# Optimization experiments

Measured on AMD Instinct MI355X. Metric: run time of the kernel, lower is better.

Reference implementation:

```python
import jax, jax.numpy as jnp
import numpy as np

N = 100000   # nodes
E = 1600000  # edges (pos and neg each)
F_IN = 256
H = 64       # hidden == out_dim


def setup_inputs() -> dict:
    key = jax.random.key(0)
    ks = jax.random.split(key, 12)
    x = jax.random.normal(ks[0], (N, F_IN), dtype=jnp.float32)
    edge_index = jax.random.randint(ks[1], (2, E), 0, N, dtype=jnp.int64)
    neg_edge_index = jax.random.randint(ks[2], (2, E), 0, N, dtype=jnp.int64)
    s = 0.05
    return {
        "x": x,
        "edge_index": edge_index,
        "neg_edge_index": neg_edge_index,
        "W1": jax.random.normal(ks[3], (F_IN, H), dtype=jnp.float32) * s,
        "b1": jnp.zeros((H,), jnp.float32),
        "W2": jax.random.normal(ks[4], (H, H), dtype=jnp.float32) * s,
        "b2": jnp.zeros((H,), jnp.float32),
        "Wp1": jax.random.normal(ks[5], (2 * H, 128), dtype=jnp.float32) * s,
        "bp1": jnp.zeros((128,), jnp.float32),
        "Wp2": jax.random.normal(ks[6], (128, 64), dtype=jnp.float32) * s,
        "bp2": jnp.zeros((64,), jnp.float32),
        "Wp3": jax.random.normal(ks[7], (64, 1), dtype=jnp.float32) * s,
        "bp3": jnp.zeros((1,), jnp.float32),
    }


def gcn_conv(x, edge_index, W, b):
    # PyG GCNConv: add self-loops, symmetric normalization D^-1/2 (A+I) D^-1/2, x@W + b
    xw = x @ W  # [N,H]
    loop = jnp.arange(N, dtype=edge_index.dtype)
    src = jnp.concatenate([edge_index[0], loop])
    dst = jnp.concatenate([edge_index[1], loop])
    deg = jax.ops.segment_sum(jnp.ones(src.shape[0], xw.dtype), dst, num_segments=N)
    dinv = jnp.where(deg > 0, jax.lax.rsqrt(jnp.maximum(deg, 1e-12)), 0.0)
    norm = dinv[src] * dinv[dst]  # [E+N]
    msgs = xw[src] * norm[:, None]
    out = jax.ops.segment_sum(msgs, dst, num_segments=N)
    return out + b


def predict_link(z, edge_index, Wp1, bp1, Wp2, bp2, Wp3, bp3):
    src, dst = edge_index[0], edge_index[1]
    # cat([z[src], z[dst]]) @ Wp1 == z[src] @ Wp1[:H] + z[dst] @ Wp1[H:]
    h = jnp.maximum(z[src] @ Wp1[:H] + z[dst] @ Wp1[H:] + bp1, 0.0)
    h = jnp.maximum(h @ Wp2 + bp2, 0.0)
    return (h @ Wp3 + bp3)[:, 0]


def reference(x, edge_index, neg_edge_index, W1, b1, W2, b2, Wp1, bp1, Wp2, bp2, Wp3, bp3):
    # encode (dropout inactive: eval mode)
    z = jnp.maximum(gcn_conv(x, edge_index, W1, b1), 0.0)
    z = jnp.maximum(gcn_conv(z, edge_index, W2, b2), 0.0)
    pos = predict_link(z, edge_index, Wp1, bp1, Wp2, bp2, Wp3, bp3)
    neg = predict_link(z, neg_edge_index, Wp1, bp1, Wp2, bp2, Wp3, bp3)
    return pos, neg, z
```

## Files before the change

### kernel.cpp

```cpp
#include <hip/hip_runtime.h>
#include <hip/hip_bf16.h>

#define NODES 100000
#define SCAN_B 200
#define CHUNK 500

typedef __attribute__((ext_vector_type(4))) float f4v;
typedef __attribute__((ext_vector_type(8))) short bfx8;
typedef __attribute__((ext_vector_type(4))) float f32x4;
typedef unsigned short ushort_t;
typedef unsigned int uint_t;

__device__ __forceinline__ ushort_t f2b(float f) {
  union { float f; uint_t u; } v; v.f = f;
  return (ushort_t)((v.u + 0x7fffu + ((v.u >> 16) & 1u)) >> 16);
}
__device__ __forceinline__ float b2f(ushort_t h) {
  union { uint_t u; float f; } v; v.u = ((uint_t)h) << 16;
  return v.f;
}
__device__ __forceinline__ uint_t pk2(float a, float b) {
  union { __hip_bfloat16 h; ushort_t u; } lo, hi;
  lo.h = __float2bfloat16(a);
  hi.h = __float2bfloat16(b);
  return (uint_t)lo.u | ((uint_t)hi.u << 16);
}

__device__ __forceinline__ int permn1(int r) {
  int t = r >> 4, g = (r >> 2) & 3, p = (r >> 1) & 1, e = r & 1;
  int w = 2 * (t & 1) + p;
  return 32 * (t >> 1) + 8 * (g ^ w) + 2 * w + e;
}

#define MFMA16(A, B, C) __builtin_amdgcn_mfma_f32_16x16x32_bf16((A), (B), (C), 0, 0, 0)


__global__ void count_deg(const int* __restrict__ dst, int* __restrict__ deg, int E) {
  int i = blockIdx.x * 256 + threadIdx.x;
  if (i < E) atomicAdd(&deg[dst[i]], 1);
}

__global__ void dinv_k(const int* __restrict__ deg, float* __restrict__ dinv, int n) {
  int i = blockIdx.x * 256 + threadIdx.x;
  if (i < n) dinv[i] = 1.0f / sqrtf((float)(deg[i] + 1));
}

__global__ void scan_sum(const int* __restrict__ deg, int* __restrict__ bsum) {
  __shared__ int sh[256];
  int b = blockIdx.x, t = threadIdx.x;
  int base = b * CHUNK;
  int v = 0;
  for (int i = t; i < CHUNK; i += 256) v += deg[base + i];
  sh[t] = v;
  __syncthreads();
  for (int s = 128; s > 0; s >>= 1) {
    if (t < s) sh[t] += sh[t + s];
    __syncthreads();
  }
  if (t == 0) bsum[b] = sh[0];
}

__global__ void scan_top(int* __restrict__ bsum) {
  __shared__ int sh[SCAN_B];
  int t = threadIdx.x;
  if (t < SCAN_B) sh[t] = bsum[t];
  __syncthreads();
  if (t == 0) {
    int run = 0;
    for (int i = 0; i < SCAN_B; ++i) { int x = sh[i]; sh[i] = run; run += x; }
  }
  __syncthreads();
  if (t < SCAN_B) bsum[t] = sh[t];
}

__global__ void scan_out(const int* __restrict__ deg, const int* __restrict__ bsum,
                         int* __restrict__ row_start, int E) {
  __shared__ int sh[CHUNK];
  int b = blockIdx.x, t = threadIdx.x;
  int base = b * CHUNK;
  for (int i = t; i < CHUNK; i += 256) sh[i] = deg[base + i];
  __syncthreads();
  if (t == 0) {
    int run = bsum[b];
    for (int i = 0; i < CHUNK; ++i) { int x = sh[i]; sh[i] = run; run += x; }
  }
  __syncthreads();
  for (int i = t; i < CHUNK; i += 256) row_start[base + i] = sh[i];
  if (b == SCAN_B - 1 && t == 0) row_start[NODES] = E;
}

__global__ void fill_csr(const int* __restrict__ src, const int* __restrict__ dst,
                         const int* __restrict__ row_start, int* __restrict__ cursor,
                         int* __restrict__ csr, int E) {
  int i = blockIdx.x * 256 + threadIdx.x;
  if (i < E) {
    int d = dst[i];
    int p = atomicAdd(&cursor[d], 1);
    csr[row_start[d] + p] = src[i];
  }
}

template <int K>
__global__ __launch_bounds__(256) void conv_gemm(
    const float* __restrict__ A, const float* __restrict__ W,
    const float* __restrict__ dinv, float* __restrict__ out, int n) {
  constexpr int KT = K / 32;
  constexpr int SEGS = K / 8;
  __shared__ __align__(16) ushort_t lhi[32 * K];
  __shared__ __align__(16) ushort_t llo[32 * K];

  int tid = threadIdx.x;
  int lane = tid & 63, wave = tid >> 6;
  int q = lane & 15, g = lane >> 4;
  int c0 = wave * 16;
  int r0 = blockIdx.x * 32;

  bfx8 bhi[KT], blo[KT];
#pragma unroll
  for (int kt = 0; kt < KT; ++kt) {
    bfx8 h, l;
#pragma unroll
    for (int j = 0; j < 8; ++j) {
      float w = W[(size_t)(kt * 32 + g * 8 + j) * 64 + c0 + q];
      ushort_t hb = f2b(w);
      float lo = w - b2f(hb);
      h[j] = (short)hb;
      l[j] = (short)f2b(lo);
    }
    bhi[kt] = h;
    blo[kt] = l;
  }

  for (int idx = tid; idx < 32 * SEGS; idx += 256) {
    int row = idx / SEGS, s = idx % SEGS;
    const float* p = A + (size_t)(r0 + row) * K + s * 8;
    f4v v0 = *(const f4v*)p;
    f4v v1 = *(const f4v*)(p + 4);
    bfx8 h8, l8;
#pragma unroll
    for (int j = 0; j < 4; ++j) {
      ushort_t hb = f2b(v0[j]);
      h8[j] = (short)hb;
      l8[j] = (short)f2b(v0[j] - b2f(hb));
      ushort_t hb1 = f2b(v1[j]);
      h8[4 + j] = (short)hb1;
      l8[4 + j] = (short)f2b(v1[j] - b2f(hb1));
    }
    int boff = row * (K * 2) + ((s * 16) ^ ((row & 7) << 4));
    *(bfx8*)((char*)lhi + boff) = h8;
    *(bfx8*)((char*)llo + boff) = l8;
  }
  __syncthreads();

  f32x4 hh[2], hl[2], lh[2];
#pragma unroll
  for (int rt = 0; rt < 2; ++rt) {
    hh[rt] = (f32x4){0.f, 0.f, 0.f, 0.f};
    hl[rt] = (f32x4){0.f, 0.f, 0.f, 0.f};
    lh[rt] = (f32x4){0.f, 0.f, 0.f, 0.f};
  }
#pragma unroll
  for (int kt = 0; kt < KT; ++kt) {
#pragma unroll
    for (int rt = 0; rt < 2; ++rt) {
      int row = rt * 16 + q;
      int boff = row * (K * 2) + (((kt * 64 + g * 16)) ^ ((row & 7) << 4));
      bfx8 ah = *(const bfx8*)((const char*)lhi + boff);
      bfx8 al = *(const bfx8*)((const char*)llo + boff);
      hh[rt] = MFMA16(ah, bhi[kt], hh[rt]);
      hl[rt] = MFMA16(ah, blo[kt], hl[rt]);
      lh[rt] = MFMA16(al, bhi[kt], lh[rt]);
    }
  }

#pragma unroll
  for (int rt = 0; rt < 2; ++rt) {
    f32x4 s = hh[rt] + hl[rt] + lh[rt];
#pragma unroll
    for (int j = 0; j < 4; ++j) {
      int row = r0 + rt * 16 + g * 4 + j;
      if (row < n) out[(size_t)row * 64 + c0 + q] = s[j] * dinv[row];
    }
  }
}

__global__ void agg_k(const float* __restrict__ P, const int* __restrict__ row_start,
                      const int* __restrict__ csr, const float* __restrict__ dinv,
                      const float* __restrict__ bias, float* __restrict__ out,
                      ushort_t* __restrict__ zb, int n) {
  int wave = threadIdx.x >> 6, lane = threadIdx.x & 63;
  int i = blockIdx.x * 4 + wave;
  if (i >= n) return;
  const float* Pl = P + lane;
  float a0 = Pl[(size_t)i * 64];
  float a1 = 0.f, a2 = 0.f, a3 = 0.f;
  int beg = row_start[i], end = row_start[i + 1];
  int j = beg;
  for (; j + 8 <= end; j += 8) {
    int s0 = csr[j + 0], s1 = csr[j + 1], s2 = csr[j + 2], s3 = csr[j + 3];
    int s4 = csr[j + 4], s5 = csr[j + 5], s6 = csr[j + 6], s7 = csr[j + 7];
    float v0 = Pl[(size_t)s0 * 64];
    float v1 = Pl[(size_t)s1 * 64];
    float v2 = Pl[(size_t)s2 * 64];
    float v3 = Pl[(size_t)s3 * 64];
    float v4 = Pl[(size_t)s4 * 64];
    float v5 = Pl[(size_t)s5 * 64];
    float v6 = Pl[(size_t)s6 * 64];
    float v7 = Pl[(size_t)s7 * 64];
    a0 += v0; a1 += v1; a2 += v2; a3 += v3;
    a0 += v4; a1 += v5; a2 += v6; a3 += v7;
  }
  if (j + 4 <= end) {
    int s0 = csr[j + 0], s1 = csr[j + 1], s2 = csr[j + 2], s3 = csr[j + 3];
    float v0 = Pl[(size_t)s0 * 64];
    float v1 = Pl[(size_t)s1 * 64];
    float v2 = Pl[(size_t)s2 * 64];
    float v3 = Pl[(size_t)s3 * 64];
    a0 += v0; a1 += v1; a2 += v2; a3 += v3;
    j += 4;
  }
  for (; j < end; ++j) a1 += Pl[(size_t)csr[j] * 64];
  float acc = (a0 + a1) + (a2 + a3);
  float v = fmaxf(acc * dinv[i] + bias[lane], 0.0f);
  out[(size_t)i * 64 + lane] = v;
  if (zb) zb[(size_t)i * 64 + lane] = f2b(v);
}

__global__ __launch_bounds__(1024) void mlp_kernel(
    const int* __restrict__ ei, const ushort_t* __restrict__ zb,
    const float* __restrict__ Wp1, const float* __restrict__ bp1,
    const float* __restrict__ Wp2, const float* __restrict__ bp2,
    const float* __restrict__ Wp3, const float* __restrict__ bp3,
    float* __restrict__ out, int E) {
  __shared__ __align__(16) char WT1[32768];
  __shared__ __align__(16) char WF2[16384];
  __shared__ __align__(16) float Lb1[128];
  __shared__ __align__(16) float Lb2[64];
  __shared__ __align__(16) float Lw3[64];

  int tid = threadIdx.x;
  int lane = tid & 63, wave = tid >> 6;
  int q = lane & 15, g = lane >> 4;

  for (int idx = tid; idx < 2048; idx += 1024) {
    int l = idx & 63, f = idx >> 6;
    int t = f & 7, kk = f >> 3;
    int lq = l & 15, lg = l >> 4;
    int n1 = permn1(t * 16 + lq);
    bfx8 v;
#pragma unroll
    for (int j = 0; j < 8; ++j)
      v[j] = (short)f2b(Wp1[(kk * 32 + lg * 8 + j) * 128 + n1]);
    *(bfx8*)(WT1 + idx * 16) = v;
  }
  for (int idx = tid; idx < 1024; idx += 1024) {
    int l = idx & 63, fk = idx >> 6;
    int t2 = fk >> 2, kk = fk & 3;
    int lq = l & 15, lg = l >> 4;
    bfx8 v;
#pragma unroll
    for (int j = 0; j < 8; ++j)
      v[j] = (short)f2b(Wp2[(kk * 32 + lg * 8 + j) * 64 + t2 * 16 + lq]);
    *(bfx8*)(WF2 + idx * 16) = v;
  }
  if (tid < 128) Lb1[tid] = bp1[permn1(tid)];
  if (tid < 64) { Lb2[tid] = bp2[tid]; Lw3[tid] = Wp3[tid]; }
  __syncthreads();

  float bp3v = bp3[0];

  int nbt = E >> 8;
  int bt0 = blockIdx.x << 2;
  int ewq = (wave << 4) + q;

  int si[6], di[6];
  bfx8 af[4], afn[4];

  {
    int e = ((bt0 + 0) < nbt) ? (((bt0 + 0) << 8) + ewq) : 0;
    si[0] = ei[e]; di[0] = ei[E + e];
  }
  {
    int e = ((bt0 + 1) < nbt) ? (((bt0 + 1) << 8) + ewq) : 0;
    si[1] = ei[e]; di[1] = ei[E + e];
  }
#pragma unroll
  for (int kk = 0; kk < 4; ++kk) {
    int node = (kk < 2) ? si[0] : di[0];
    af[kk] = *(const bfx8*)(zb + (size_t)node * 64 + ((kk & 1) << 5) + (g << 3));
  }

#pragma unroll
  for (int it = 0; it < 4; ++it) {
    if (bt0 + it < nbt) {
      if (it + 2 < 4) {
        int e = ((bt0 + it + 2) < nbt) ? (((bt0 + it + 2) << 8) + ewq) : 0;
        si[it + 2] = ei[e]; di[it + 2] = ei[E + e];
      }
      if (it + 1 < 4 && (bt0 + it + 1) < nbt) {
#pragma unroll
        for (int kk = 0; kk < 4; ++kk) {
          int node = (kk < 2) ? si[it + 1] : di[it + 1];
          afn[kk] = *(const bfx8*)(zb + (size_t)node * 64 + ((kk & 1) << 5) + (g << 3));
        }
      } else {
#pragma unroll
        for (int kk = 0; kk < 4; ++kk) afn[kk] = af[kk];
      }

      f32x4 acc2[4];
#pragma unroll
      for (int t2 = 0; t2 < 4; ++t2) acc2[t2] = (f32x4){0.f, 0.f, 0.f, 0.f};

#pragma unroll
      for (int m = 0; m < 4; ++m) {
        f32x4 a0 = (f32x4){0.f, 0.f, 0.f, 0.f};
        f32x4 a1 = (f32x4){0.f, 0.f, 0.f, 0.f};
#pragma unroll
        for (int kk = 0; kk < 4; ++kk) {
          bfx8 wf0 = *(const bfx8*)(WT1 + ((kk * 8 + 2 * m) * 64 + lane) * 16);
          bfx8 wf1 = *(const bfx8*)(WT1 + ((kk * 8 + 2 * m + 1) * 64 + lane) * 16);
          a0 = MFMA16(wf0, af[kk], a0);
          a1 = MFMA16(wf1, af[kk], a1);
        }
        f4v bv0 = *(const f4v*)(Lb1 + (2 * m) * 16 + g * 4);
        f4v bv1 = *(const f4v*)(Lb1 + (2 * m + 1) * 16 + g * 4);
        bfx8 wf2[4];
#pragma unroll
        for (int t2 = 0; t2 < 4; ++t2)
          wf2[t2] = *(const bfx8*)(WF2 + ((t2 * 4 + m) * 64 + lane) * 16);
        uint_t c0 = pk2(fmaxf(a0[0] + bv0[0], 0.f), fmaxf(a0[1] + bv0[1], 0.f));
        uint_t c1 = pk2(fmaxf(a0[2] + bv0[2], 0.f), fmaxf(a0[3] + bv0[3], 0.f));
        uint_t c2 = pk2(fmaxf(a1[0] + bv1[0], 0.f), fmaxf(a1[1] + bv1[1], 0.f));
        uint_t c3 = pk2(fmaxf(a1[2] + bv1[2], 0.f), fmaxf(a1[3] + bv1[3], 0.f));
        uint_t d1 = __shfl_xor(c1, 16, 64);
        uint_t d2 = __shfl_xor(c2, 32, 64);
        uint_t d3 = __shfl_xor(c3, 48, 64);
        union { uint_t u[4]; bfx8 v; } hf;
        hf.u[0] = c0; hf.u[1] = d1; hf.u[2] = d2; hf.u[3] = d3;
#pragma unroll
        for (int t2 = 0; t2 < 4; ++t2)
          acc2[t2] = MFMA16(wf2[t2], hf.v, acc2[t2]);
      }

      float sacc = 0.f;
#pragma unroll
      for (int t2 = 0; t2 < 4; ++t2) {
        f4v b2v = *(const f4v*)(Lb2 + t2 * 16 + g * 4);
        f4v w3v = *(const f4v*)(Lw3 + t2 * 16 + g * 4);
#pragma unroll
        for (int j = 0; j < 4; ++j) {
          float h = fmaxf(acc2[t2][j] + b2v[j], 0.f);
          sacc = fmaf(h, w3v[j], sacc);
        }
      }
      sacc += __shfl_xor(sacc, 16, 64);
      sacc += __shfl_xor(sacc, 32, 64);
      if (g == 0) out[((bt0 + it) << 8) + ewq] = sacc + bp3v;

#pragma unroll
      for (int kk = 0; kk < 4; ++kk) af[kk] = afn[kk];
    }
  }
}


static inline size_t alup(size_t x) { return (x + 511) & ~(size_t)511; }

extern "C" void kernel_launch(void* const* d_in, const int* in_sizes, int n_in,
                              void* d_out, int out_size, void* d_ws, size_t ws_size,
                              hipStream_t stream) {
  const float* x = (const float*)d_in[0];
  const int* ei = (const int*)d_in[1];
  const int* nei = (const int*)d_in[2];
  const float* W1 = (const float*)d_in[3];
  const float* b1 = (const float*)d_in[4];
  const float* W2 = (const float*)d_in[5];
  const float* b2 = (const float*)d_in[6];
  const float* Wp1 = (const float*)d_in[7];
  const float* bp1 = (const float*)d_in[8];
  const float* Wp2 = (const float*)d_in[9];
  const float* bp2 = (const float*)d_in[10];
  const float* Wp3 = (const float*)d_in[11];
  const float* bp3 = (const float*)d_in[12];

  const int N = NODES;
  const int E = in_sizes[1] / 2;

  float* pos = (float*)d_out;
  float* neg = pos + E;
  float* z = pos + (size_t)2 * E;

  char* w = (char*)d_ws;
  size_t off = 0;
  int* deg = (int*)(w + off); off = alup(off + (size_t)N * 4);
  int* cur = (int*)(w + off); off = alup(off + (size_t)N * 4);
  float* dinv = (float*)(w + off); off = alup(off + (size_t)N * 4);
  int* bsum = (int*)(w + off); off = alup(off + 256 * 4);
  int* row_start = (int*)(w + off); off = alup(off + (size_t)(N + 1) * 4);
  int* csr = (int*)(w + off); off = alup(off + (size_t)E * 4);
  float* xw = (float*)(w + off); off = alup(off + (size_t)N * 64 * 4);
  float* z1 = (float*)(w + off); off = alup(off + (size_t)N * 64 * 4);
  ushort_t* zb = (ushort_t*)(w + off); off = alup(off + (size_t)N * 64 * 2);

  hipMemsetAsync(deg, 0, (size_t)N * 4, stream);
  hipMemsetAsync(cur, 0, (size_t)N * 4, stream);

  count_deg<<<(E + 255) / 256, 256, 0, stream>>>(ei + E, deg, E);
  dinv_k<<<(N + 255) / 256, 256, 0, stream>>>(deg, dinv, N);
  scan_sum<<<SCAN_B, 256, 0, stream>>>(deg, bsum);
  scan_top<<<1, 256, 0, stream>>>(bsum);
  scan_out<<<SCAN_B, 256, 0, stream>>>(deg, bsum, row_start, E);
  fill_csr<<<(E + 255) / 256, 256, 0, stream>>>(ei, ei + E, row_start, cur, csr, E);

  conv_gemm<256><<<(N + 31) / 32, 256, 0, stream>>>(x, W1, dinv, xw, N);
  agg_k<<<(N + 3) / 4, 256, 0, stream>>>(xw, row_start, csr, dinv, b1, z1, nullptr, N);
  conv_gemm<64><<<(N + 31) / 32, 256, 0, stream>>>(z1, W2, dinv, xw, N);
  agg_k<<<(N + 3) / 4, 256, 0, stream>>>(xw, row_start, csr, dinv, b2, z, zb, N);

  int nbt = E >> 8;
  int grid = (nbt + 3) / 4;
  mlp_kernel<<<grid, 1024, 0, stream>>>(ei, zb, Wp1, bp1, Wp2, bp2, Wp3, bp3, pos, E);
  mlp_kernel<<<grid, 1024, 0, stream>>>(nei, zb, Wp1, bp1, Wp2, bp2, Wp3, bp3, neg, E);
}
```

Before: 562.3 us.

## Vectorize GCN aggregation to float4 per lane and merge pos/neg MLP launches

The aggregation kernel now handles four nodes per wave, with 16 lanes per node each loading a float4. This cuts the number of gather instructions per edge and keeps more independent rows in flight. The positive and negative link-prediction MLPs are merged into a single launch of twice the grid, with each block picking its edge list and output by block index. This removes one launch and the tail gap between the two kernels, at the cost of less unrolling per node in the aggregation loop.

```diff
diff --git a/kernel.cpp b/kernel.cpp
--- a/kernel.cpp
+++ b/kernel.cpp
@@ -8,6 +8,7 @@
 typedef __attribute__((ext_vector_type(4))) float f4v;
 typedef __attribute__((ext_vector_type(8))) short bfx8;
 typedef __attribute__((ext_vector_type(4))) float f32x4;
+typedef __attribute__((ext_vector_type(4))) unsigned short us4v;
 typedef unsigned short ushort_t;
 typedef unsigned int uint_t;
 
@@ -189,49 +190,52 @@
                       const float* __restrict__ bias, float* __restrict__ out,
                       ushort_t* __restrict__ zb, int n) {
   int wave = threadIdx.x >> 6, lane = threadIdx.x & 63;
-  int i = blockIdx.x * 4 + wave;
+  int r = lane >> 4;
+  int c = (lane & 15) << 2;
+  int i = (blockIdx.x * 4 + wave) * 4 + r;
   if (i >= n) return;
-  const float* Pl = P + lane;
-  float a0 = Pl[(size_t)i * 64];
-  float a1 = 0.f, a2 = 0.f, a3 = 0.f;
+
+  const float* Pc = P + c;
+  f4v a0 = *(const f4v*)(Pc + (size_t)i * 64);
+  f4v a1 = (f4v){0.f, 0.f, 0.f, 0.f};
+  f4v a2 = (f4v){0.f, 0.f, 0.f, 0.f};
+  f4v a3 = (f4v){0.f, 0.f, 0.f, 0.f};
+
   int beg = row_start[i], end = row_start[i + 1];
   int j = beg;
-  for (; j + 8 <= end; j += 8) {
+  for (; j + 4 <= end; j += 4) {
     int s0 = csr[j + 0], s1 = csr[j + 1], s2 = csr[j + 2], s3 = csr[j + 3];
-    int s4 = csr[j + 4], s5 = csr[j + 5], s6 = csr[j + 6], s7 = csr[j + 7];
-    float v0 = Pl[(size_t)s0 * 64];
-    float v1 = Pl[(size_t)s1 * 64];
-    float v2 = Pl[(size_t)s2 * 64];
-    float v3 = Pl[(size_t)s3 * 64];
-    float v4 = Pl[(size_t)s4 * 64];
-    float v5 = Pl[(size_t)s5 * 64];
-    float v6 = Pl[(size_t)s6 * 64];
-    float v7 = Pl[(size_t)s7 * 64];
+    f4v v0 = *(const f4v*)(Pc + (size_t)s0 * 64);
+    f4v v1 = *(const f4v*)(Pc + (size_t)s1 * 64);
+    f4v v2 = *(const f4v*)(Pc + (size_t)s2 * 64);
+    f4v v3 = *(const f4v*)(Pc + (size_t)s3 * 64);
     a0 += v0; a1 += v1; a2 += v2; a3 += v3;
-    a0 += v4; a1 += v5; a2 += v6; a3 += v7;
-  }
-  if (j + 4 <= end) {
-    int s0 = csr[j + 0], s1 = csr[j + 1], s2 = csr[j + 2], s3 = csr[j + 3];
-    float v0 = Pl[(size_t)s0 * 64];
-    float v1 = Pl[(size_t)s1 * 64];
-    float v2 = Pl[(size_t)s2 * 64];
-    float v3 = Pl[(size_t)s3 * 64];
-    a0 += v0; a1 += v1; a2 += v2; a3 += v3;
-    j += 4;
-  }
-  for (; j < end; ++j) a1 += Pl[(size_t)csr[j] * 64];
-  float acc = (a0 + a1) + (a2 + a3);
-  float v = fmaxf(acc * dinv[i] + bias[lane], 0.0f);
-  out[(size_t)i * 64 + lane] = v;
-  if (zb) zb[(size_t)i * 64 + lane] = f2b(v);
+  }
+  for (; j < end; ++j) a1 += *(const f4v*)(Pc + (size_t)csr[j] * 64);
+
+  f4v acc = (a0 + a1) + (a2 + a3);
+  float di = dinv[i];
+  f4v bv = *(const f4v*)(bias + c);
+  f4v v;
+#pragma unroll
+  for (int k = 0; k < 4; ++k) v[k] = fmaxf(acc[k] * di + bv[k], 0.0f);
+  *(f4v*)(out + (size_t)i * 64 + c) = v;
+  if (zb) {
+    us4v h;
+#pragma unroll
+    for (int k = 0; k < 4; ++k) h[k] = f2b(v[k]);
+    *(us4v*)(zb + (size_t)i * 64 + c) = h;
+  }
 }
 
 __global__ __launch_bounds__(1024) void mlp_kernel(
-    const int* __restrict__ ei, const ushort_t* __restrict__ zb,
+    const int* __restrict__ ei, const int* __restrict__ nei,
+    const ushort_t* __restrict__ zb,
     const float* __restrict__ Wp1, const float* __restrict__ bp1,
     const float* __restrict__ Wp2, const float* __restrict__ bp2,
     const float* __restrict__ Wp3, const float* __restrict__ bp3,
-    float* __restrict__ out, int E) {
+    float* __restrict__ pos, float* __restrict__ neg,
+    int E, int gridHalf) {
   __shared__ __align__(16) char WT1[32768];
   __shared__ __align__(16) char WF2[16384];
   __shared__ __align__(16) float Lb1[128];
@@ -269,8 +273,13 @@
 
   float bp3v = bp3[0];
 
+  int side = (blockIdx.x >= gridHalf) ? 1 : 0;
+  const int* eip = side ? nei : ei;
+  float* outp = side ? neg : pos;
+  int bb = blockIdx.x - side * gridHalf;
+
   int nbt = E >> 8;
-  int bt0 = blockIdx.x << 2;
+  int bt0 = bb << 2;
   int ewq = (wave << 4) + q;
 
   int si[6], di[6];
@@ -278,11 +287,11 @@
 
   {
     int e = ((bt0 + 0) < nbt) ? (((bt0 + 0) << 8) + ewq) : 0;
-    si[0] = ei[e]; di[0] = ei[E + e];
+    si[0] = eip[e]; di[0] = eip[E + e];
   }
   {
     int e = ((bt0 + 1) < nbt) ? (((bt0 + 1) << 8) + ewq) : 0;
-    si[1] = ei[e]; di[1] = ei[E + e];
+    si[1] = eip[e]; di[1] = eip[E + e];
   }
 #pragma unroll
   for (int kk = 0; kk < 4; ++kk) {
@@ -295,7 +304,7 @@
     if (bt0 + it < nbt) {
       if (it + 2 < 4) {
         int e = ((bt0 + it + 2) < nbt) ? (((bt0 + it + 2) << 8) + ewq) : 0;
-        si[it + 2] = ei[e]; di[it + 2] = ei[E + e];
+        si[it + 2] = eip[e]; di[it + 2] = eip[E + e];
       }
       if (it + 1 < 4 && (bt0 + it + 1) < nbt) {
 #pragma unroll
@@ -356,7 +365,7 @@
       }
       sacc += __shfl_xor(sacc, 16, 64);
       sacc += __shfl_xor(sacc, 32, 64);
-      if (g == 0) out[((bt0 + it) << 8) + ewq] = sacc + bp3v;
+      if (g == 0) outp[((bt0 + it) << 8) + ewq] = sacc + bp3v;
 
 #pragma unroll
       for (int kk = 0; kk < 4; ++kk) af[kk] = afn[kk];
@@ -414,12 +423,12 @@
   fill_csr<<<(E + 255) / 256, 256, 0, stream>>>(ei, ei + E, row_start, cur, csr, E);
 
   conv_gemm<256><<<(N + 31) / 32, 256, 0, stream>>>(x, W1, dinv, xw, N);
-  agg_k<<<(N + 3) / 4, 256, 0, stream>>>(xw, row_start, csr, dinv, b1, z1, nullptr, N);
+  agg_k<<<(N + 15) / 16, 256, 0, stream>>>(xw, row_start, csr, dinv, b1, z1, nullptr, N);
   conv_gemm<64><<<(N + 31) / 32, 256, 0, stream>>>(z1, W2, dinv, xw, N);
-  agg_k<<<(N + 3) / 4, 256, 0, stream>>>(xw, row_start, csr, dinv, b2, z, zb, N);
+  agg_k<<<(N + 15) / 16, 256, 0, stream>>>(xw, row_start, csr, dinv, b2, z, zb, N);
 
   int nbt = E >> 8;
-  int grid = (nbt + 3) / 4;
-  mlp_kernel<<<grid, 1024, 0, stream>>>(ei, zb, Wp1, bp1, Wp2, bp2, Wp3, bp3, pos, E);
-  mlp_kernel<<<grid, 1024, 0, stream>>>(nei, zb, Wp1, bp1, Wp2, bp2, Wp3, bp3, neg, E);
-}
+  int gridHalf = (nbt + 3) / 4;
+  mlp_kernel<<<2 * gridHalf, 1024, 0, stream>>>(ei, nei, zb, Wp1, bp1, Wp2, bp2,
+                                                Wp3, bp3, pos, neg, E, gridHalf);
+}
```

New measurement: 566.1 us. About the same (+0.7%).
